# Performance work log

Measured on AMD Instinct MI355X. Metric: run time of the kernel, lower is better.

## Reference

```python
import jax, jax.numpy as jnp
import numpy as np

N = 100000      # nodes
E = 3200000     # edges (avg degree 32)
F = 256         # input features
C = 256         # output channels


def setup_inputs() -> dict:
    key = jax.random.key(0)
    k1, k2, k3, k4, k5 = jax.random.split(key, 5)
    x = jax.random.normal(k1, (N, F), dtype=jnp.float32)
    edge_row = jax.random.randint(k2, (E,), 0, N, dtype=jnp.int32)
    edge_col = jax.random.randint(k3, (E,), 0, N, dtype=jnp.int32)
    # precomputed normalized adjacency values (D^-1/2 (A+I) D^-1/2 entries)
    edge_vals = jax.random.uniform(k4, (E,), dtype=jnp.float32)
    kernel = jax.random.normal(k5, (F, C), dtype=jnp.float32) * (1.0 / np.sqrt(F))
    bias = jnp.zeros((C,), dtype=jnp.float32)
    return {"x": x, "edge_row": edge_row, "edge_col": edge_col,
            "edge_vals": edge_vals, "kernel": kernel, "bias": bias}


def reference(x, edge_row, edge_col, edge_vals, kernel, bias):
    # GraphConv: Z = relu( A_hat @ (X @ W) + b ), single mode, sparse A_hat.
    h = x @ kernel                                   # [N, C]
    msgs = edge_vals[:, None] * h[edge_col]          # [E, C] gather along cols
    agg = jax.ops.segment_sum(msgs, edge_row, num_segments=N)  # [N, C]
    return jax.nn.relu(agg + bias)
```

## Files before the change

kernel.cpp:

```cpp
#include <hip/hip_runtime.h>
#include <hip/hip_bf16.h>
#include <hip/hip_fp16.h>


#define CAP 2432
#define NBMAX 1600
#define CH_A3 8192
#define D1_SMEM 19200

typedef __attribute__((ext_vector_type(4))) float f32x4;
typedef __attribute__((ext_vector_type(8))) short s16x8;

__device__ __forceinline__ unsigned short f2bf(float f) {
    unsigned u = __float_as_uint(f);
    u += 0x7FFFu + ((u >> 16) & 1u);
    return (unsigned short)(u >> 16);
}
__device__ __forceinline__ float bf2f(unsigned short s) {
    return __uint_as_float(((unsigned)s) << 16);
}

__global__ __launch_bounds__(256) void k_pre(const float* __restrict__ W,
                                             unsigned short* __restrict__ Wt,
                                             int* __restrict__ gcur, int NB) {
    int bid = blockIdx.x, t = threadIdx.x;
    if (bid < 256) {
        int idx = bid * 256 + t;
        int k = idx >> 8, c = idx & 255;
        Wt[c * 256 + k] = f2bf(W[idx]);
    } else {
        for (int j = t; j < NB; j += 256) gcur[j] = 0;
    }
}

__device__ __forceinline__ void a3_body(const int* __restrict__ row,
                                        const int* __restrict__ col,
                                        const float* __restrict__ val,
                                        int* __restrict__ gcur,
                                        int2* __restrict__ bin8,
                                        int E, int NB, int chunk, char* smem) {
    int* h    = (int*)smem;
    int* base = h + NBMAX;
    int* cur  = base + NBMAX;
    int t = threadIdx.x;
    for (int j = t; j < NB; j += 256) { h[j] = 0; cur[j] = 0; }
    __syncthreads();
    int start = chunk * CH_A3;
    int end = min(E, start + CH_A3);
    for (int i = start + t; i < end; i += 256)
        atomicAdd(&h[row[i] >> 6], 1);
    __syncthreads();
    for (int j = t; j < NB; j += 256) {
        int c = h[j];
        base[j] = c ? atomicAdd(&gcur[j], c) : 0;
    }
    __syncthreads();
    for (int i = start + t; i < end; i += 256) {
        int r = row[i];
        int b = r >> 6;
        int ofs = atomicAdd(&cur[b], 1);
        unsigned hb = (unsigned)__half_as_ushort(__float2half(val[i]));
        bin8[(size_t)b * CAP + base[b] + ofs] =
            make_int2((int)((unsigned)col[i] | (hb << 17)), r & 63);
    }
}

__device__ __forceinline__ void gemm_body(const float* __restrict__ X,
                                          const unsigned short* __restrict__ Wt,
                                          unsigned short* __restrict__ H,
                                          int M, int g, char* smem) {
    typedef unsigned short AsRow[40];
    AsRow* As = (AsRow*)smem;
    int t = threadIdx.x;
    int lane = t & 63;
    int w = t >> 6;
    int r0 = g * 64;
    int c0 = w * 64;
    int srow = t >> 2;
    int sslot = t & 3;
    int gr = r0 + srow; if (gr >= M) gr = M - 1;

    f32x4 acc[4][4] = {};

    for (int k0 = 0; k0 < 256; k0 += 32) {
        const float* p = &X[(size_t)gr * 256 + k0 + sslot * 8];
        f32x4 a0 = __builtin_nontemporal_load((const f32x4*)p);
        f32x4 a1 = __builtin_nontemporal_load((const f32x4*)(p + 4));
        s16x8 va;
        va[0] = (short)f2bf(a0[0]); va[1] = (short)f2bf(a0[1]);
        va[2] = (short)f2bf(a0[2]); va[3] = (short)f2bf(a0[3]);
        va[4] = (short)f2bf(a1[0]); va[5] = (short)f2bf(a1[1]);
        va[6] = (short)f2bf(a1[2]); va[7] = (short)f2bf(a1[3]);
        __syncthreads();
        *(s16x8*)&As[srow][sslot * 8] = va;
        __syncthreads();

        int kofs = (lane >> 4) * 8;
        s16x8 afr[4], bfr[4];
#pragma unroll
        for (int mi = 0; mi < 4; ++mi)
            afr[mi] = *(const s16x8*)&As[mi * 16 + (lane & 15)][kofs];
#pragma unroll
        for (int ni = 0; ni < 4; ++ni) {
            int cn = c0 + ni * 16 + (lane & 15);
            bfr[ni] = *(const s16x8*)&Wt[(size_t)cn * 256 + k0 + kofs];
        }
#pragma unroll
        for (int mi = 0; mi < 4; ++mi)
#pragma unroll
            for (int ni = 0; ni < 4; ++ni)
                acc[mi][ni] = __builtin_amdgcn_mfma_f32_16x16x32_bf16(
                    afr[mi], bfr[ni], acc[mi][ni], 0, 0, 0);
    }

#pragma unroll
    for (int mi = 0; mi < 4; ++mi) {
#pragma unroll
        for (int ni = 0; ni < 4; ++ni) {
            int rg = r0 + mi * 16 + (lane >> 4) * 4;
            int cg = c0 + ni * 16 + (lane & 15);
#pragma unroll
            for (int j = 0; j < 4; ++j) {
                if (rg + j < M)
                    H[(size_t)(rg + j) * 256 + cg] = f2bf(acc[mi][ni][j]);
            }
        }
    }
}

__global__ __launch_bounds__(256) void kD1(const int* __restrict__ row,
                                           const int* __restrict__ col,
                                           const float* __restrict__ val,
                                           int* __restrict__ gcur,
                                           int2* __restrict__ bin8,
                                           int E, int NB, int nA3,
                                           const float* __restrict__ X,
                                           const unsigned short* __restrict__ Wt,
                                           unsigned short* __restrict__ H, int M) {
    extern __shared__ char smem[];
    int bid = blockIdx.x;
    if (bid < nA3) {
        a3_body(row, col, val, gcur, bin8, E, NB, bid, smem);
        return;
    }
    gemm_body(X, Wt, H, M, bid - nA3, smem);
}

__global__ __launch_bounds__(256) void kB2(int2* __restrict__ bin8,
                                           const int* __restrict__ gcur,
                                           int2* __restrict__ rowinfo, int N) {
    __shared__ int2 se[CAP];
    __shared__ int hist[4][64];
    __shared__ int rs[64], cnt[64];
    int b = blockIdx.x;
    int t = threadIdx.x;
    int w = t >> 6;
    size_t gb = (size_t)b * CAP;
    int n = gcur[b];

    if (t < 64) { hist[0][t] = 0; hist[1][t] = 0; hist[2][t] = 0; hist[3][t] = 0; }
    __syncthreads();
    for (int i = t; i < n; i += 256) {
        int2 e = bin8[gb + i];
        se[i] = e;
        atomicAdd(&hist[w][e.y], 1);
    }
    __syncthreads();
    if (t < 64) {
        int h0 = hist[0][t], h1 = hist[1][t], h2 = hist[2][t], h3 = hist[3][t];
        cnt[t] = h0 + h1 + h2 + h3;
        rs[t] = cnt[t];
        hist[0][t] = 0;
        hist[1][t] = h0;
        hist[2][t] = h0 + h1;
        hist[3][t] = h0 + h1 + h2;
    }
    __syncthreads();
    for (int off = 1; off < 64; off <<= 1) {
        int v = (t < 64 && t >= off) ? rs[t - off] : 0;
        __syncthreads();
        if (t < 64 && t >= off) rs[t] += v;
        __syncthreads();
    }
    unsigned* cvout = (unsigned*)&bin8[gb];
    if (t < 64) {
        int st = rs[t] - cnt[t];
        hist[0][t] += st; hist[1][t] += st;
        hist[2][t] += st; hist[3][t] += st;
        int node = b * 64 + t;
        if (node < N) rowinfo[node] = make_int2((int)(gb * 2 + st), cnt[t]);
    }
    __syncthreads();
    for (int i = t; i < n; i += 256) {
        int2 e = se[i];
        int pos = atomicAdd(&hist[w][e.y], 1);
        cvout[pos] = (unsigned)e.x;
    }
}

__global__ __launch_bounds__(256) void k_agg(const unsigned short* __restrict__ H,
                                             const int2* __restrict__ rowinfo,
                                             const unsigned* __restrict__ csr,
                                             const float* __restrict__ bias,
                                             float* __restrict__ out, int n) {
    int wave = threadIdx.x >> 6;
    int lane = threadIdx.x & 63;
    int node = blockIdx.x * 4 + wave;
    if (node >= n) return;
    int2 ri = rowinfo[node];
    int s = ri.x;
    int e = ri.x + ri.y;
    int h = lane >> 5;
    int cbase = (lane & 31) * 8;

    float a0=0.f,a1=0.f,a2=0.f,a3=0.f,a4=0.f,a5=0.f,a6=0.f,a7=0.f;

#define ACC(K, HV)                                                      \
    {                                                                   \
        float v = __half2float(__ushort_as_half((unsigned short)((K) >> 17))); \
        a0 += v * bf2f((unsigned short)(HV)[0]);                        \
        a1 += v * bf2f((unsigned short)(HV)[1]);                        \
        a2 += v * bf2f((unsigned short)(HV)[2]);                        \
        a3 += v * bf2f((unsigned short)(HV)[3]);                        \
        a4 += v * bf2f((unsigned short)(HV)[4]);                        \
        a5 += v * bf2f((unsigned short)(HV)[5]);                        \
        a6 += v * bf2f((unsigned short)(HV)[6]);                        \
        a7 += v * bf2f((unsigned short)(HV)[7]);                        \
    }

    int i = s;
    for (; i + 7 < e; i += 8) {
        unsigned k0 = csr[i + h];
        unsigned k1 = csr[i + 2 + h];
        unsigned k2 = csr[i + 4 + h];
        unsigned k3 = csr[i + 6 + h];
        s16x8 g0 = *(const s16x8*)&H[(k0 & 0x1FFFFu) * 256 + cbase];
        s16x8 g1 = *(const s16x8*)&H[(k1 & 0x1FFFFu) * 256 + cbase];
        s16x8 g2 = *(const s16x8*)&H[(k2 & 0x1FFFFu) * 256 + cbase];
        s16x8 g3 = *(const s16x8*)&H[(k3 & 0x1FFFFu) * 256 + cbase];
        ACC(k0, g0); ACC(k1, g1); ACC(k2, g2); ACC(k3, g3);
    }
    for (; i + 1 < e; i += 2) {
        unsigned k0 = csr[i + h];
        s16x8 g0 = *(const s16x8*)&H[(k0 & 0x1FFFFu) * 256 + cbase];
        ACC(k0, g0);
    }
    if (i < e) {
        unsigned k0 = csr[i];
        s16x8 g0 = *(const s16x8*)&H[(k0 & 0x1FFFFu) * 256 + cbase];
        float v = h ? 0.f
                    : __half2float(__ushort_as_half((unsigned short)(k0 >> 17)));
        a0 += v * bf2f((unsigned short)g0[0]);
        a1 += v * bf2f((unsigned short)g0[1]);
        a2 += v * bf2f((unsigned short)g0[2]);
        a3 += v * bf2f((unsigned short)g0[3]);
        a4 += v * bf2f((unsigned short)g0[4]);
        a5 += v * bf2f((unsigned short)g0[5]);
        a6 += v * bf2f((unsigned short)g0[6]);
        a7 += v * bf2f((unsigned short)g0[7]);
    }
#undef ACC

    a0 += __shfl_xor(a0, 32); a1 += __shfl_xor(a1, 32);
    a2 += __shfl_xor(a2, 32); a3 += __shfl_xor(a3, 32);
    a4 += __shfl_xor(a4, 32); a5 += __shfl_xor(a5, 32);
    a6 += __shfl_xor(a6, 32); a7 += __shfl_xor(a7, 32);

    float w0 = h ? a4 : a0;
    float w1 = h ? a5 : a1;
    float w2 = h ? a6 : a2;
    float w3 = h ? a7 : a3;
    int cw = cbase + h * 4;
    float4 b4 = *(const float4*)&bias[cw];
    float4 o;
    o.x = fmaxf(w0 + b4.x, 0.f);
    o.y = fmaxf(w1 + b4.y, 0.f);
    o.z = fmaxf(w2 + b4.z, 0.f);
    o.w = fmaxf(w3 + b4.w, 0.f);
    *(float4*)&out[(size_t)node * 256 + cw] = o;
}

extern "C" void kernel_launch(void* const* d_in, const int* in_sizes, int n_in,
                              void* d_out, int out_size, void* d_ws, size_t ws_size,
                              hipStream_t stream) {
    const float* x     = (const float*)d_in[0];
    const int*   erow  = (const int*)d_in[1];
    const int*   ecol  = (const int*)d_in[2];
    const float* evals = (const float*)d_in[3];
    const float* W     = (const float*)d_in[4];
    const float* bias  = (const float*)d_in[5];
    float* out = (float*)d_out;

    const int C = 256;
    const int N = in_sizes[0] / C;
    const int E = in_sizes[1];
    const int NB = (N + 63) / 64;

    char* ws = (char*)d_ws;
    size_t off = 0;
    auto carve = [&](size_t bytes) -> void* {
        void* p = ws + off;
        off += (bytes + 255) & ~(size_t)255;
        return p;
    };
    unsigned short* Hbf = (unsigned short*)carve((size_t)N * C * 2);
    unsigned short* Wt  = (unsigned short*)carve((size_t)C * 256 * 2);
    int*            gcur= (int*)carve((size_t)NB * 4);
    int2*           rinf= (int2*)carve((size_t)N * 8);
    int2*           bin8= (int2*)carve((size_t)NB * CAP * 8);

    int nA3 = (E + CH_A3 - 1) / CH_A3;
    int gemmBlocks = (N + 63) / 64;

    k_pre<<<257, 256, 0, stream>>>(W, Wt, gcur, NB);
    kD1<<<nA3 + gemmBlocks, 256, D1_SMEM, stream>>>(erow, ecol, evals, gcur,
                                                    bin8, E, NB, nA3,
                                                    x, Wt, Hbf, N);
    kB2<<<NB, 256, 0, stream>>>(bin8, gcur, rinf, N);
    k_agg<<<(N + 3) / 4, 256, 0, stream>>>(Hbf, rinf, (unsigned*)bin8, bias, out, N);
}
```

Measured before the change: 362.0 us.

## Split GEMM blocks across binning and CSR-build launches to overlap work

The dense X@W GEMM blocks were all co-launched with the edge-binning kernel. Now only the first 1000 GEMM tiles run there, and the remaining tiles run alongside the per-bucket CSR sort (formerly kB2, now kD2 with dynamic shared memory). The goal is to balance the two launches so the latency-bound sort phase overlaps useful GEMM work. The cost is a fixed split constant that may not balance well, and larger dynamic shared memory for the sort blocks.

```diff
diff --git a/kernel.cpp b/kernel.cpp
--- a/kernel.cpp
+++ b/kernel.cpp
@@ -7,6 +7,8 @@
 #define NBMAX 1600
 #define CH_A3 8192
 #define D1_SMEM 19200
+#define D2_SMEM 20992
+#define G1SPLIT 1000
 
 typedef __attribute__((ext_vector_type(4))) float f32x4;
 typedef __attribute__((ext_vector_type(8))) short s16x8;
@@ -128,6 +130,59 @@
     }
 }
 
+__device__ __forceinline__ void kb2_body(int2* __restrict__ bin8,
+                                         const int* __restrict__ gcur,
+                                         int2* __restrict__ rowinfo,
+                                         int N, int b, char* smem) {
+    int2* se  = (int2*)smem;
+    int* hist = (int*)(se + CAP);
+    int* rs   = hist + 256;
+    int* cnt  = rs + 64;
+    int t = threadIdx.x;
+    int w = t >> 6;
+    size_t gb = (size_t)b * CAP;
+    int n = gcur[b];
+
+    if (t < 64) { hist[0*64+t] = 0; hist[1*64+t] = 0; hist[2*64+t] = 0; hist[3*64+t] = 0; }
+    __syncthreads();
+    for (int i = t; i < n; i += 256) {
+        int2 e = bin8[gb + i];
+        se[i] = e;
+        atomicAdd(&hist[w*64 + e.y], 1);
+    }
+    __syncthreads();
+    if (t < 64) {
+        int h0 = hist[0*64+t], h1 = hist[1*64+t], h2 = hist[2*64+t], h3 = hist[3*64+t];
+        cnt[t] = h0 + h1 + h2 + h3;
+        rs[t] = cnt[t];
+        hist[0*64+t] = 0;
+        hist[1*64+t] = h0;
+        hist[2*64+t] = h0 + h1;
+        hist[3*64+t] = h0 + h1 + h2;
+    }
+    __syncthreads();
+    for (int off = 1; off < 64; off <<= 1) {
+        int v = (t < 64 && t >= off) ? rs[t - off] : 0;
+        __syncthreads();
+        if (t < 64 && t >= off) rs[t] += v;
+        __syncthreads();
+    }
+    unsigned* cvout = (unsigned*)&bin8[gb];
+    if (t < 64) {
+        int st = rs[t] - cnt[t];
+        hist[0*64+t] += st; hist[1*64+t] += st;
+        hist[2*64+t] += st; hist[3*64+t] += st;
+        int node = b * 64 + t;
+        if (node < N) rowinfo[node] = make_int2((int)(gb * 2 + st), cnt[t]);
+    }
+    __syncthreads();
+    for (int i = t; i < n; i += 256) {
+        int2 e = se[i];
+        int pos = atomicAdd(&hist[w*64 + e.y], 1);
+        cvout[pos] = (unsigned)e.x;
+    }
+}
+
 __global__ __launch_bounds__(256) void kD1(const int* __restrict__ row,
                                            const int* __restrict__ col,
                                            const float* __restrict__ val,
@@ -146,56 +201,21 @@
     gemm_body(X, Wt, H, M, bid - nA3, smem);
 }
 
-__global__ __launch_bounds__(256) void kB2(int2* __restrict__ bin8,
+__global__ __launch_bounds__(256) void kD2(int2* __restrict__ bin8,
                                            const int* __restrict__ gcur,
-                                           int2* __restrict__ rowinfo, int N) {
-    __shared__ int2 se[CAP];
-    __shared__ int hist[4][64];
-    __shared__ int rs[64], cnt[64];
-    int b = blockIdx.x;
-    int t = threadIdx.x;
-    int w = t >> 6;
-    size_t gb = (size_t)b * CAP;
-    int n = gcur[b];
-
-    if (t < 64) { hist[0][t] = 0; hist[1][t] = 0; hist[2][t] = 0; hist[3][t] = 0; }
-    __syncthreads();
-    for (int i = t; i < n; i += 256) {
-        int2 e = bin8[gb + i];
-        se[i] = e;
-        atomicAdd(&hist[w][e.y], 1);
-    }
-    __syncthreads();
-    if (t < 64) {
-        int h0 = hist[0][t], h1 = hist[1][t], h2 = hist[2][t], h3 = hist[3][t];
-        cnt[t] = h0 + h1 + h2 + h3;
-        rs[t] = cnt[t];
-        hist[0][t] = 0;
-        hist[1][t] = h0;
-        hist[2][t] = h0 + h1;
-        hist[3][t] = h0 + h1 + h2;
-    }
-    __syncthreads();
-    for (int off = 1; off < 64; off <<= 1) {
-        int v = (t < 64 && t >= off) ? rs[t - off] : 0;
-        __syncthreads();
-        if (t < 64 && t >= off) rs[t] += v;
-        __syncthreads();
-    }
-    unsigned* cvout = (unsigned*)&bin8[gb];
-    if (t < 64) {
-        int st = rs[t] - cnt[t];
-        hist[0][t] += st; hist[1][t] += st;
-        hist[2][t] += st; hist[3][t] += st;
-        int node = b * 64 + t;
-        if (node < N) rowinfo[node] = make_int2((int)(gb * 2 + st), cnt[t]);
-    }
-    __syncthreads();
-    for (int i = t; i < n; i += 256) {
-        int2 e = se[i];
-        int pos = atomicAdd(&hist[w][e.y], 1);
-        cvout[pos] = (unsigned)e.x;
-    }
+                                           int2* __restrict__ rowinfo,
+                                           int N, int NB,
+                                           const float* __restrict__ X,
+                                           const unsigned short* __restrict__ Wt,
+                                           unsigned short* __restrict__ H,
+                                           int M, int g0) {
+    extern __shared__ char smem[];
+    int bid = blockIdx.x;
+    if (bid < NB) {
+        kb2_body(bin8, gcur, rowinfo, N, bid, smem);
+        return;
+    }
+    gemm_body(X, Wt, H, M, g0 + (bid - NB), smem);
 }
 
 __global__ __launch_bounds__(256) void k_agg(const unsigned short* __restrict__ H,
@@ -311,11 +331,14 @@
 
     int nA3 = (E + CH_A3 - 1) / CH_A3;
     int gemmBlocks = (N + 63) / 64;
+    int G1 = G1SPLIT;
+    int G2 = gemmBlocks - G1;
 
     k_pre<<<257, 256, 0, stream>>>(W, Wt, gcur, NB);
-    kD1<<<nA3 + gemmBlocks, 256, D1_SMEM, stream>>>(erow, ecol, evals, gcur,
-                                                    bin8, E, NB, nA3,
-                                                    x, Wt, Hbf, N);
-    kB2<<<NB, 256, 0, stream>>>(bin8, gcur, rinf, N);
+    kD1<<<nA3 + G1, 256, D1_SMEM, stream>>>(erow, ecol, evals, gcur,
+                                            bin8, E, NB, nA3,
+                                            x, Wt, Hbf, N);
+    kD2<<<NB + G2, 256, D2_SMEM, stream>>>(bin8, gcur, rinf, N, NB,
+                                           x, Wt, Hbf, N, G1);
     k_agg<<<(N + 3) / 4, 256, 0, stream>>>(Hbf, rinf, (unsigned*)bin8, bias, out, N);
 }
```

Measured after the change: 385.2 us. 6.4% more time.
